# Kernel optimization log

Hardware: AMD Instinct MI355X
Metric: run time of the kernel (lower is better)

Reference implementation:

```python
import jax, jax.numpy as jnp
import numpy as np

N_NODES = 100000
N_EDGES = 1600000
IN_DIM = 128
HID = 32
HEADS = 4
OUT_DIM = 32


def gat_conv(x, W, al, ar, b, src, dst, apply_elu):
    """DGL-style GATConv. x:[N,F_in], W:[F_in,H*D], al/ar/b:[H,D]."""
    N = x.shape[0]
    H, D = al.shape
    f = (x @ W).reshape(N, H, D)                      # projected features [N,H,D]
    el = jnp.sum(f * al, axis=-1)                     # [N,H]
    er = jnp.sum(f * ar, axis=-1)                     # [N,H]
    e = jax.nn.leaky_relu(el[src] + er[dst], 0.2)     # per-edge scores [E,H]
    # segment softmax over incoming edges of each dst node
    m = jax.ops.segment_max(e, dst, num_segments=N)   # [N,H]
    m = jnp.where(jnp.isfinite(m), m, 0.0)            # zero-in-degree safety
    w = jnp.exp(e - m[dst])                           # [E,H]
    s = jax.ops.segment_sum(w, dst, num_segments=N)   # [N,H]
    alpha = w / jnp.maximum(s[dst], 1e-9)             # [E,H]
    out = jax.ops.segment_sum(alpha[:, :, None] * f[src], dst, num_segments=N)  # [N,H,D]
    out = out + b
    if apply_elu:
        out = jax.nn.elu(out)
    return out


def setup_inputs() -> dict:
    key = jax.random.key(0)
    ks = jax.random.split(key, 16)
    sc = 0.05
    HD = HEADS * HID
    return {
        "x": jax.random.normal(ks[0], (N_NODES, IN_DIM), jnp.float32),
        "src": jax.random.randint(ks[1], (N_EDGES,), 0, N_NODES, jnp.int32),
        "dst": jax.random.randint(ks[2], (N_EDGES,), 0, N_NODES, jnp.int32),
        "W1": jax.random.normal(ks[3], (IN_DIM, HD), jnp.float32) * sc,
        "al1": jax.random.normal(ks[4], (HEADS, HID), jnp.float32) * sc,
        "ar1": jax.random.normal(ks[5], (HEADS, HID), jnp.float32) * sc,
        "b1": jnp.zeros((HEADS, HID), jnp.float32),
        "W2": jax.random.normal(ks[6], (HD, HD), jnp.float32) * sc,
        "al2": jax.random.normal(ks[7], (HEADS, HID), jnp.float32) * sc,
        "ar2": jax.random.normal(ks[8], (HEADS, HID), jnp.float32) * sc,
        "b2": jnp.zeros((HEADS, HID), jnp.float32),
        "W3": jax.random.normal(ks[9], (HD, OUT_DIM), jnp.float32) * sc,
        "al3": jax.random.normal(ks[10], (1, OUT_DIM), jnp.float32) * sc,
        "ar3": jax.random.normal(ks[11], (1, OUT_DIM), jnp.float32) * sc,
        "b3": jnp.zeros((1, OUT_DIM), jnp.float32),
    }


def reference(x, src, dst, W1, al1, ar1, b1, W2, al2, ar2, b2, W3, al3, ar3, b3):
    h = gat_conv(x, W1, al1, ar1, b1, src, dst, apply_elu=True)
    h = h.reshape(h.shape[0], -1)                     # concat heads [N, H*D]
    h = gat_conv(h, W2, al2, ar2, b2, src, dst, apply_elu=True)
    h = h.reshape(h.shape[0], -1)
    h = gat_conv(h, W3, al3, ar3, b3, src, dst, apply_elu=False)
    return h.squeeze(1)                               # [N, OUT_DIM]
```

## Files before the change

kernel.cpp:

```cpp
#include <hip/hip_runtime.h>
#include <hip/hip_bf16.h>

#define IN_DIM 128
#define HDIM 128

typedef __attribute__((ext_vector_type(8))) short bf16x8;
typedef __attribute__((ext_vector_type(4))) float f32x4;
typedef __attribute__((ext_vector_type(4))) unsigned short ushort4v;

__device__ __forceinline__ float bf2f(unsigned short h) {
  union { unsigned u; float f; } a; a.u = ((unsigned)h) << 16; return a.f;
}
__device__ __forceinline__ unsigned short f2bf(float x) {
  union { float f; unsigned u; } a; a.f = x;
  unsigned r = a.u + 0x7FFFu + ((a.u >> 16) & 1u);
  return (unsigned short)(r >> 16);
}
__device__ __forceinline__ void bfsplit(float x, unsigned short& h, unsigned short& l) {
  h = f2bf(x);
  l = f2bf(x - bf2f(h));
}


__global__ __launch_bounds__(256) void hist_kernel(const int* __restrict__ dst,
                                                   int* __restrict__ deg, int E) {
  int e = blockIdx.x * 256 + threadIdx.x;
  if (e < E) atomicAdd(&deg[dst[e]], 1);
}

__global__ __launch_bounds__(512) void scan1_kernel(const int* __restrict__ deg,
                                                    int* __restrict__ partial,
                                                    int* __restrict__ bsum, int n) {
  __shared__ int sm[512];
  int g = blockIdx.x * 512 + threadIdx.x;
  int v = (g < n) ? deg[g] : 0;
  sm[threadIdx.x] = v;
  __syncthreads();
  for (int off = 1; off < 512; off <<= 1) {
    int t = (threadIdx.x >= off) ? sm[threadIdx.x - off] : 0;
    __syncthreads();
    sm[threadIdx.x] += t;
    __syncthreads();
  }
  if (g < n) partial[g] = sm[threadIdx.x];
  if (threadIdx.x == 511) bsum[blockIdx.x] = sm[511];
}

__global__ __launch_bounds__(512) void scan2_kernel(int* __restrict__ bsum, int nblk) {
  __shared__ int sm[512];
  int v = (threadIdx.x < nblk) ? bsum[threadIdx.x] : 0;
  sm[threadIdx.x] = v;
  __syncthreads();
  for (int off = 1; off < 512; off <<= 1) {
    int t = (threadIdx.x >= off) ? sm[threadIdx.x - off] : 0;
    __syncthreads();
    sm[threadIdx.x] += t;
    __syncthreads();
  }
  if (threadIdx.x < nblk) bsum[threadIdx.x] = sm[threadIdx.x];
}

__global__ __launch_bounds__(512) void scanfix_kernel(const int* __restrict__ partial,
                                                      const int* __restrict__ bsum,
                                                      const int* __restrict__ deg,
                                                      int* __restrict__ row_ptr,
                                                      int* __restrict__ cursor, int n) {
  int g = blockIdx.x * 512 + threadIdx.x;
  if (g >= n) return;
  int off = (blockIdx.x > 0) ? bsum[blockIdx.x - 1] : 0;
  int incl = partial[g] + off;
  row_ptr[g + 1] = incl;
  cursor[g] = incl - deg[g];
  if (g == 0) row_ptr[0] = 0;
}

__global__ __launch_bounds__(256) void scatter_kernel(const int* __restrict__ src,
                                                      const int* __restrict__ dst,
                                                      int* __restrict__ cursor,
                                                      int* __restrict__ col, int E) {
  int e = blockIdx.x * 256 + threadIdx.x;
  if (e >= E) return;
  int d = dst[e];
  int p = atomicAdd(&cursor[d], 1);
  col[p] = src[e];
}


__global__ __launch_bounds__(256) void split_kernel(const float* __restrict__ x,
                                                    unsigned short* __restrict__ xhi,
                                                    unsigned short* __restrict__ xlo,
                                                    int total4) {
  int idx = blockIdx.x * 256 + threadIdx.x;
  if (idx >= total4) return;
  float4 v = *(const float4*)&x[(size_t)idx * 4];
  ushort4v h, l;
  unsigned short a, b;
  bfsplit(v.x, a, b); h.x = a; l.x = b;
  bfsplit(v.y, a, b); h.y = a; l.y = b;
  bfsplit(v.z, a, b); h.z = a; l.z = b;
  bfsplit(v.w, a, b); h.w = a; l.w = b;
  *(ushort4v*)&xhi[(size_t)idx * 4] = h;
  *(ushort4v*)&xlo[(size_t)idx * 4] = l;
}


__global__ __launch_bounds__(64) void wfrag_kernel(const float* __restrict__ W, int HD, int NB,
                                                   unsigned short* __restrict__ whi,
                                                   unsigned short* __restrict__ wlo) {
  int fb = blockIdx.x;
  int l = threadIdx.x;
  int kb = fb / NB, nb = fb % NB;
  unsigned short hi[8], lo[8];
#pragma unroll
  for (int j = 0; j < 8; ++j) {
    int k = kb * 32 + (l >> 4) * 8 + j;
    int c = nb * 16 + (l & 15);
    bfsplit(W[(size_t)k * HD + c], hi[j], lo[j]);
  }
  size_t off = ((size_t)fb * 64 + l) * 8;
#pragma unroll
  for (int j = 0; j < 8; ++j) { whi[off + j] = hi[j]; wlo[off + j] = lo[j]; }
}


__global__ __launch_bounds__(256) void gemm128_mfma_kernel(
    const unsigned short* __restrict__ xhi, const unsigned short* __restrict__ xlo,
    const unsigned short* __restrict__ whi, const unsigned short* __restrict__ wlo,
    const float* __restrict__ al, const float* __restrict__ ar,
    float* __restrict__ F, float* __restrict__ el, float* __restrict__ er, int n) {
  const int lane = threadIdx.x & 63;
  const int w = threadIdx.x >> 6;
  const int bm = blockIdx.x * 128;
  const int lr = lane & 15;
  const int lk = lane >> 4;

  f32x4 acc[2][8];
#pragma unroll
  for (int mf = 0; mf < 2; ++mf)
#pragma unroll
    for (int nb = 0; nb < 8; ++nb) acc[mf][nb] = (f32x4){0.f, 0.f, 0.f, 0.f};

  int arow[2];
#pragma unroll
  for (int mf = 0; mf < 2; ++mf) {
    int r = bm + w * 32 + mf * 16 + lr;
    arow[mf] = (r < n) ? r : (n - 1);
  }

  for (int kb = 0; kb < 4; ++kb) {
    bf16x8 ah[2], alo2[2];
#pragma unroll
    for (int mf = 0; mf < 2; ++mf) {
      size_t ab = (size_t)arow[mf] * 128 + kb * 32 + lk * 8;
      ah[mf] = *(const bf16x8*)(xhi + ab);
      alo2[mf] = *(const bf16x8*)(xlo + ab);
    }
#pragma unroll
    for (int nb = 0; nb < 8; ++nb) {
      size_t wb = ((size_t)(kb * 8 + nb) * 64 + lane) * 8;
      bf16x8 bh = *(const bf16x8*)(whi + wb);
      bf16x8 bl = *(const bf16x8*)(wlo + wb);
#pragma unroll
      for (int mf = 0; mf < 2; ++mf) {
        acc[mf][nb] = __builtin_amdgcn_mfma_f32_16x16x32_bf16(ah[mf], bh, acc[mf][nb], 0, 0, 0);
        acc[mf][nb] = __builtin_amdgcn_mfma_f32_16x16x32_bf16(ah[mf], bl, acc[mf][nb], 0, 0, 0);
        acc[mf][nb] = __builtin_amdgcn_mfma_f32_16x16x32_bf16(alo2[mf], bh, acc[mf][nb], 0, 0, 0);
      }
    }
  }

  float alv[4][2], arv[4][2];
#pragma unroll
  for (int hh = 0; hh < 4; ++hh)
#pragma unroll
    for (int p = 0; p < 2; ++p) {
      alv[hh][p] = al[hh * 32 + p * 16 + lr];
      arv[hh][p] = ar[hh * 32 + p * 16 + lr];
    }

#pragma unroll
  for (int mf = 0; mf < 2; ++mf) {
#pragma unroll
    for (int r = 0; r < 4; ++r) {
      int grow = bm + w * 32 + mf * 16 + lk * 4 + r;
      bool ok = grow < n;
      if (ok) {
#pragma unroll
        for (int nb = 0; nb < 8; ++nb)
          F[(size_t)grow * HDIM + nb * 16 + lr] = acc[mf][nb][r];
      }
#pragma unroll
      for (int hh = 0; hh < 4; ++hh) {
        float pl = acc[mf][2 * hh][r] * alv[hh][0] + acc[mf][2 * hh + 1][r] * alv[hh][1];
        float pr = acc[mf][2 * hh][r] * arv[hh][0] + acc[mf][2 * hh + 1][r] * arv[hh][1];
        pl += __shfl_xor(pl, 1); pl += __shfl_xor(pl, 2);
        pl += __shfl_xor(pl, 4); pl += __shfl_xor(pl, 8);
        pr += __shfl_xor(pr, 1); pr += __shfl_xor(pr, 2);
        pr += __shfl_xor(pr, 4); pr += __shfl_xor(pr, 8);
        if (ok && lr == 0) {
          el[grow * 4 + hh] = pl;
          er[grow * 4 + hh] = pr;
        }
      }
    }
  }
}


__global__ __launch_bounds__(256) void gemm_n32_kernel(const unsigned short* __restrict__ Xhi,
                                                       const unsigned short* __restrict__ Xlo,
                                                       const float* __restrict__ W,
                                                       const float* __restrict__ al,
                                                       const float* __restrict__ ar,
                                                       float* __restrict__ Fout,
                                                       float* __restrict__ el,
                                                       float* __restrict__ er, int n) {
  __shared__ float Xs[32][132];
  __shared__ float Ws[128][32];
  const int tid = threadIdx.x;
  const int row0 = blockIdx.x * 32;
#pragma unroll
  for (int jj = 0; jj < 4; ++jj) {
    int idx = tid + jj * 256;
    int r = idx >> 3;
    int c4 = (idx & 7) * 4;
    *(float4*)&Ws[r][c4] = *(const float4*)&W[(size_t)r * 32 + c4];
  }
#pragma unroll
  for (int jj = 0; jj < 4; ++jj) {
    int idx = tid + jj * 256;
    int r = idx >> 5;
    int c4 = (idx & 31) * 4;
    int row = row0 + r;
    if (row < n) {
      ushort4v h = *(const ushort4v*)&Xhi[(size_t)row * HDIM + c4];
      ushort4v l = *(const ushort4v*)&Xlo[(size_t)row * HDIM + c4];
      Xs[r][c4 + 0] = bf2f(h.x) + bf2f(l.x);
      Xs[r][c4 + 1] = bf2f(h.y) + bf2f(l.y);
      Xs[r][c4 + 2] = bf2f(h.z) + bf2f(l.z);
      Xs[r][c4 + 3] = bf2f(h.w) + bf2f(l.w);
    } else {
      Xs[r][c4 + 0] = 0.f; Xs[r][c4 + 1] = 0.f; Xs[r][c4 + 2] = 0.f; Xs[r][c4 + 3] = 0.f;
    }
  }
  __syncthreads();
  const int r = tid >> 3, cg = (tid & 7) * 4;
  float4 acc = make_float4(0.f, 0.f, 0.f, 0.f);
#pragma unroll 8
  for (int k = 0; k < 128; ++k) {
    float a = Xs[r][k];
    float4 b = *(const float4*)&Ws[k][cg];
    acc.x = fmaf(a, b.x, acc.x); acc.y = fmaf(a, b.y, acc.y);
    acc.z = fmaf(a, b.z, acc.z); acc.w = fmaf(a, b.w, acc.w);
  }
  int row = row0 + r;
  if (row < n) *(float4*)&Fout[(size_t)row * 32 + cg] = acc;
  float pl = acc.x * al[cg] + acc.y * al[cg + 1] + acc.z * al[cg + 2] + acc.w * al[cg + 3];
  float pr = acc.x * ar[cg] + acc.y * ar[cg + 1] + acc.z * ar[cg + 2] + acc.w * ar[cg + 3];
  pl += __shfl_xor(pl, 1); pl += __shfl_xor(pl, 2); pl += __shfl_xor(pl, 4);
  pr += __shfl_xor(pr, 1); pr += __shfl_xor(pr, 2); pr += __shfl_xor(pr, 4);
  if ((tid & 7) == 0 && row < n) { el[row] = pl; er[row] = pr; }
}


template <int H, int D, bool ELU, bool OSPLIT>
__global__ __launch_bounds__(256) void aggregate_kernel(const float* __restrict__ f,
                                                        const float* __restrict__ el,
                                                        const float* __restrict__ er,
                                                        const float* __restrict__ bias,
                                                        const int* __restrict__ row_ptr,
                                                        const int* __restrict__ col,
                                                        float* __restrict__ out,
                                                        unsigned short* __restrict__ ohi,
                                                        unsigned short* __restrict__ olo,
                                                        int n) {
  constexpr int F = H * D;
  constexpr int LPN = F / 4;
  constexpr int NPB = 256 / LPN;
  int node = blockIdx.x * NPB + threadIdx.x / LPN;
  int ll = threadIdx.x % LPN;
  if (node >= n) return;
  const int h = (4 * ll) / D;
  const float er_n = er[node * H + h];
  int beg = row_ptr[node], end = row_ptr[node + 1];

  float ssum = 0.f;
  float4 acc = make_float4(0.f, 0.f, 0.f, 0.f);

  constexpr int U = 8;
  int i = beg;
  for (; i + U <= end; i += U) {
    int s[U];
#pragma unroll
    for (int j = 0; j < U; ++j) s[j] = col[i + j];
    float4 fv[U];
#pragma unroll
    for (int j = 0; j < U; ++j) fv[j] = *(const float4*)&f[(size_t)s[j] * F + 4 * ll];
    float elv[U];
#pragma unroll
    for (int j = 0; j < U; ++j) elv[j] = el[s[j] * H + h];
#pragma unroll
    for (int j = 0; j < U; ++j) {
      float e = elv[j] + er_n;
      e = (e > 0.f) ? e : 0.2f * e;
      float wgt = __expf(e);
      ssum += wgt;
      acc.x = fmaf(wgt, fv[j].x, acc.x);
      acc.y = fmaf(wgt, fv[j].y, acc.y);
      acc.z = fmaf(wgt, fv[j].z, acc.z);
      acc.w = fmaf(wgt, fv[j].w, acc.w);
    }
  }
  for (; i < end; ++i) {
    int s = col[i];
    float e = el[s * H + h] + er_n;
    e = (e > 0.f) ? e : 0.2f * e;
    float wgt = __expf(e);
    float4 fv = *(const float4*)&f[(size_t)s * F + 4 * ll];
    ssum += wgt;
    acc.x = fmaf(wgt, fv.x, acc.x);
    acc.y = fmaf(wgt, fv.y, acc.y);
    acc.z = fmaf(wgt, fv.z, acc.z);
    acc.w = fmaf(wgt, fv.w, acc.w);
  }

  float inv = 1.f / fmaxf(ssum, 1e-9f);
  float4 bb = *(const float4*)&bias[4 * ll];
  float4 o;
  o.x = acc.x * inv + bb.x;
  o.y = acc.y * inv + bb.y;
  o.z = acc.z * inv + bb.z;
  o.w = acc.w * inv + bb.w;
  if (ELU) {
    o.x = (o.x > 0.f) ? o.x : (__expf(o.x) - 1.f);
    o.y = (o.y > 0.f) ? o.y : (__expf(o.y) - 1.f);
    o.z = (o.z > 0.f) ? o.z : (__expf(o.z) - 1.f);
    o.w = (o.w > 0.f) ? o.w : (__expf(o.w) - 1.f);
  }
  if (OSPLIT) {
    ushort4v hi, lo;
    unsigned short a, b;
    bfsplit(o.x, a, b); hi.x = a; lo.x = b;
    bfsplit(o.y, a, b); hi.y = a; lo.y = b;
    bfsplit(o.z, a, b); hi.z = a; lo.z = b;
    bfsplit(o.w, a, b); hi.w = a; lo.w = b;
    *(ushort4v*)&ohi[(size_t)node * F + 4 * ll] = hi;
    *(ushort4v*)&olo[(size_t)node * F + 4 * ll] = lo;
  } else {
    *(float4*)&out[(size_t)node * F + 4 * ll] = o;
  }
}


extern "C" void kernel_launch(void* const* d_in, const int* in_sizes, int n_in,
                              void* d_out, int out_size, void* d_ws, size_t ws_size,
                              hipStream_t stream) {
  const float* x   = (const float*)d_in[0];
  const int*   src = (const int*)d_in[1];
  const int*   dst = (const int*)d_in[2];
  const float* W1  = (const float*)d_in[3];
  const float* al1 = (const float*)d_in[4];
  const float* ar1 = (const float*)d_in[5];
  const float* b1  = (const float*)d_in[6];
  const float* W2  = (const float*)d_in[7];
  const float* al2 = (const float*)d_in[8];
  const float* ar2 = (const float*)d_in[9];
  const float* b2  = (const float*)d_in[10];
  const float* W3  = (const float*)d_in[11];
  const float* al3 = (const float*)d_in[12];
  const float* ar3 = (const float*)d_in[13];
  const float* b3  = (const float*)d_in[14];
  float* out = (float*)d_out;

  const int N = in_sizes[0] / IN_DIM;
  const int E = in_sizes[1];

  char* w = (char*)d_ws;
  size_t off = 0;
  auto alloc = [&](size_t bytes) -> void* {
    void* p = w + off;
    off += (bytes + 255) & ~(size_t)255;
    return p;
  };
  int*   deg     = (int*)alloc((size_t)N * 4);
  int*   row_ptr = (int*)alloc((size_t)(N + 1) * 4);
  int*   cursor  = (int*)alloc((size_t)N * 4);
  int*   bsum    = (int*)alloc(4096);
  int*   col     = (int*)alloc((size_t)E * 4);
  float* el      = (float*)alloc((size_t)N * 4 * 4);
  float* er      = (float*)alloc((size_t)N * 4 * 4);
  float* bufA    = (float*)alloc((size_t)N * 128 * 4);
  unsigned short* bhi = (unsigned short*)alloc((size_t)N * 128 * 2);
  unsigned short* blo = (unsigned short*)alloc((size_t)N * 128 * 2);
  unsigned short* w1hi = (unsigned short*)alloc(4 * 8 * 64 * 8 * 2);
  unsigned short* w1lo = (unsigned short*)alloc(4 * 8 * 64 * 8 * 2);
  unsigned short* w2hi = (unsigned short*)alloc(4 * 8 * 64 * 8 * 2);
  unsigned short* w2lo = (unsigned short*)alloc(4 * 8 * 64 * 8 * 2);

  wfrag_kernel<<<32, 64, 0, stream>>>(W1, HDIM, 8, w1hi, w1lo);
  wfrag_kernel<<<32, 64, 0, stream>>>(W2, HDIM, 8, w2hi, w2lo);
  split_kernel<<<(N * 128 / 4 + 255) / 256, 256, 0, stream>>>(x, bhi, blo, N * 128 / 4);

  hipMemsetAsync(deg, 0, (size_t)N * 4, stream);
  hist_kernel<<<(E + 255) / 256, 256, 0, stream>>>(dst, deg, E);
  int nblk = (N + 511) / 512;
  scan1_kernel<<<nblk, 512, 0, stream>>>(deg, cursor, bsum, N);
  scan2_kernel<<<1, 512, 0, stream>>>(bsum, nblk);
  scanfix_kernel<<<nblk, 512, 0, stream>>>(cursor, bsum, deg, row_ptr, cursor, N);
  scatter_kernel<<<(E + 255) / 256, 256, 0, stream>>>(src, dst, cursor, col, E);

  const int gb = (N + 127) / 128;
  gemm128_mfma_kernel<<<gb, 256, 0, stream>>>(bhi, blo, w1hi, w1lo, al1, ar1, bufA, el, er, N);
  aggregate_kernel<4, 32, true, true><<<(N + 7) / 8, 256, 0, stream>>>(
      bufA, el, er, b1, row_ptr, col, nullptr, bhi, blo, N);
  gemm128_mfma_kernel<<<gb, 256, 0, stream>>>(bhi, blo, w2hi, w2lo, al2, ar2, bufA, el, er, N);
  aggregate_kernel<4, 32, true, true><<<(N + 7) / 8, 256, 0, stream>>>(
      bufA, el, er, b2, row_ptr, col, nullptr, bhi, blo, N);
  gemm_n32_kernel<<<(N + 31) / 32, 256, 0, stream>>>(bhi, blo, W3, al3, ar3, bufA, el, er, N);
  aggregate_kernel<1, 32, false, false><<<(N + 31) / 32, 256, 0, stream>>>(
      bufA, el, er, b3, row_ptr, col, out, nullptr, nullptr, N);
}
```

Baseline: 726.9 us.

## Build CSR via two-level bucketed counting sort instead of global atomics

Replaces the per-node histogram, three-kernel scan and atomic scatter with a bucketed radix-style CSR build. Edges are first grouped into 512-node buckets using shared-memory histograms and local scans, then each bucket is finalized in shared memory to produce row_ptr and col. This removes most global atomics on random addresses and several launches. It also merges the two weight-fragment kernels into one launch. It adds a temporary E-sized buffer, and the packed record format assumes src fits in 23 bits and at most 256 buckets.

```diff
diff --git a/kernel.cpp b/kernel.cpp
--- a/kernel.cpp
+++ b/kernel.cpp
@@ -3,6 +3,11 @@
 
 #define IN_DIM 128
 #define HDIM 128
+
+#define BSH 9
+#define NBKT_MAX 256
+#define CHUNK 4096
+#define EPT 16
 
 typedef __attribute__((ext_vector_type(8))) short bf16x8;
 typedef __attribute__((ext_vector_type(4))) float f32x4;
@@ -22,67 +27,139 @@
 }
 
 
-__global__ __launch_bounds__(256) void hist_kernel(const int* __restrict__ dst,
-                                                   int* __restrict__ deg, int E) {
-  int e = blockIdx.x * 256 + threadIdx.x;
-  if (e < E) atomicAdd(&deg[dst[e]], 1);
-}
-
-__global__ __launch_bounds__(512) void scan1_kernel(const int* __restrict__ deg,
-                                                    int* __restrict__ partial,
-                                                    int* __restrict__ bsum, int n) {
-  __shared__ int sm[512];
-  int g = blockIdx.x * 512 + threadIdx.x;
-  int v = (g < n) ? deg[g] : 0;
-  sm[threadIdx.x] = v;
+__global__ __launch_bounds__(256) void bhist_kernel(const int* __restrict__ dst,
+                                                    int* __restrict__ bcnt, int E, int nbkt) {
+  __shared__ int h[NBKT_MAX];
+  for (int i = threadIdx.x; i < nbkt; i += 256) h[i] = 0;
+  __syncthreads();
+  int stride = gridDim.x * 256;
+  for (int e = blockIdx.x * 256 + threadIdx.x; e < E; e += stride)
+    atomicAdd(&h[dst[e] >> BSH], 1);
+  __syncthreads();
+  for (int i = threadIdx.x; i < nbkt; i += 256)
+    if (h[i]) atomicAdd(&bcnt[i], h[i]);
+}
+
+__global__ __launch_bounds__(256) void bscan_kernel(const int* __restrict__ bcnt,
+                                                    int* __restrict__ bbase,
+                                                    int* __restrict__ bcursor,
+                                                    int* __restrict__ row_ptr, int nbkt) {
+  __shared__ int sc[256];
+  int t = threadIdx.x;
+  int v = (t < nbkt) ? bcnt[t] : 0;
+  sc[t] = v;
+  __syncthreads();
+  for (int off = 1; off < 256; off <<= 1) {
+    int u = (t >= off) ? sc[t - off] : 0;
+    __syncthreads();
+    sc[t] += u;
+    __syncthreads();
+  }
+  if (t < nbkt) { bbase[t] = sc[t] - v; bcursor[t] = 0; }
+  if (t == 0) row_ptr[0] = 0;
+}
+
+__global__ __launch_bounds__(256) void bscatter_kernel(const int* __restrict__ src,
+                                                       const int* __restrict__ dst,
+                                                       const int* __restrict__ bbase,
+                                                       int* __restrict__ bcursor,
+                                                       unsigned int* __restrict__ tmp,
+                                                       int E, int nbkt) {
+  __shared__ int cnt[NBKT_MAX];
+  __shared__ int boff[NBKT_MAX];
+  __shared__ int gb[NBKT_MAX];
+  __shared__ int sc[256];
+  __shared__ unsigned int recs[CHUNK];
+  __shared__ unsigned char bkts[CHUNK];
+  const int t = threadIdx.x;
+  for (int i = t; i < nbkt; i += 256) cnt[i] = 0;
+  __syncthreads();
+  const int base = blockIdx.x * CHUNK;
+  unsigned int myrec[EPT];
+  unsigned short myr[EPT];
+  unsigned char myb[EPT];
+#pragma unroll
+  for (int i = 0; i < EPT; ++i) {
+    int e = base + t + i * 256;
+    if (e < E) {
+      int s = src[e], d = dst[e];
+      int b = d >> BSH;
+      myb[i] = (unsigned char)b;
+      myrec[i] = ((unsigned)s << BSH) | (unsigned)(d & ((1 << BSH) - 1));
+      myr[i] = (unsigned short)atomicAdd(&cnt[b], 1);
+    } else {
+      myb[i] = 0xFF;
+    }
+  }
+  __syncthreads();
+  int cv = (t < nbkt) ? cnt[t] : 0;
+  sc[t] = cv;
+  __syncthreads();
+  for (int off = 1; off < 256; off <<= 1) {
+    int u = (t >= off) ? sc[t - off] : 0;
+    __syncthreads();
+    sc[t] += u;
+    __syncthreads();
+  }
+  if (t < nbkt) boff[t] = sc[t] - cv;
+  __syncthreads();
+  if (t < nbkt && cv > 0) gb[t] = atomicAdd(&bcursor[t], cv);
+  __syncthreads();
+#pragma unroll
+  for (int i = 0; i < EPT; ++i) {
+    if (myb[i] != 0xFF) {
+      int p = boff[myb[i]] + (int)myr[i];
+      recs[p] = myrec[i];
+      bkts[p] = myb[i];
+    }
+  }
+  __syncthreads();
+  int total = sc[255];
+  for (int i = t; i < total; i += 256) {
+    int b = bkts[i];
+    tmp[bbase[b] + gb[b] + (i - boff[b])] = recs[i];
+  }
+}
+
+__global__ __launch_bounds__(512) void bfinal_kernel(const unsigned int* __restrict__ tmp,
+                                                     const int* __restrict__ bbase,
+                                                     const int* __restrict__ bcnt,
+                                                     int* __restrict__ row_ptr,
+                                                     int* __restrict__ col, int n) {
+  const int b = blockIdx.x;
+  const int base = bbase[b];
+  const int cnt = bcnt[b];
+  const int node0 = b << BSH;
+  __shared__ int ncnt[512];
+  __shared__ int sc2[512];
+  __shared__ int cur[512];
+  const int t = threadIdx.x;
+  ncnt[t] = 0;
+  __syncthreads();
+  for (int i = t; i < cnt; i += 512) {
+    unsigned rec = tmp[base + i];
+    atomicAdd(&ncnt[rec & ((1 << BSH) - 1)], 1);
+  }
+  __syncthreads();
+  int v = ncnt[t];
+  sc2[t] = v;
   __syncthreads();
   for (int off = 1; off < 512; off <<= 1) {
-    int t = (threadIdx.x >= off) ? sm[threadIdx.x - off] : 0;
+    int u = (t >= off) ? sc2[t - off] : 0;
     __syncthreads();
-    sm[threadIdx.x] += t;
+    sc2[t] += u;
     __syncthreads();
   }
-  if (g < n) partial[g] = sm[threadIdx.x];
-  if (threadIdx.x == 511) bsum[blockIdx.x] = sm[511];
-}
-
-__global__ __launch_bounds__(512) void scan2_kernel(int* __restrict__ bsum, int nblk) {
-  __shared__ int sm[512];
-  int v = (threadIdx.x < nblk) ? bsum[threadIdx.x] : 0;
-  sm[threadIdx.x] = v;
-  __syncthreads();
-  for (int off = 1; off < 512; off <<= 1) {
-    int t = (threadIdx.x >= off) ? sm[threadIdx.x - off] : 0;
-    __syncthreads();
-    sm[threadIdx.x] += t;
-    __syncthreads();
-  }
-  if (threadIdx.x < nblk) bsum[threadIdx.x] = sm[threadIdx.x];
-}
-
-__global__ __launch_bounds__(512) void scanfix_kernel(const int* __restrict__ partial,
-                                                      const int* __restrict__ bsum,
-                                                      const int* __restrict__ deg,
-                                                      int* __restrict__ row_ptr,
-                                                      int* __restrict__ cursor, int n) {
-  int g = blockIdx.x * 512 + threadIdx.x;
-  if (g >= n) return;
-  int off = (blockIdx.x > 0) ? bsum[blockIdx.x - 1] : 0;
-  int incl = partial[g] + off;
-  row_ptr[g + 1] = incl;
-  cursor[g] = incl - deg[g];
-  if (g == 0) row_ptr[0] = 0;
-}
-
-__global__ __launch_bounds__(256) void scatter_kernel(const int* __restrict__ src,
-                                                      const int* __restrict__ dst,
-                                                      int* __restrict__ cursor,
-                                                      int* __restrict__ col, int E) {
-  int e = blockIdx.x * 256 + threadIdx.x;
-  if (e >= E) return;
-  int d = dst[e];
-  int p = atomicAdd(&cursor[d], 1);
-  col[p] = src[e];
+  cur[t] = base + sc2[t] - v;
+  int node = node0 + t;
+  if (node < n) row_ptr[node + 1] = base + sc2[t];
+  __syncthreads();
+  for (int i = t; i < cnt; i += 512) {
+    unsigned rec = tmp[base + i];
+    int ln = rec & ((1 << BSH) - 1);
+    int p = atomicAdd(&cur[ln], 1);
+    col[p] = (int)(rec >> BSH);
+  }
 }
 
 
@@ -104,18 +181,24 @@
 }
 
 
-__global__ __launch_bounds__(64) void wfrag_kernel(const float* __restrict__ W, int HD, int NB,
-                                                   unsigned short* __restrict__ whi,
-                                                   unsigned short* __restrict__ wlo) {
-  int fb = blockIdx.x;
+__global__ __launch_bounds__(64) void wfrag_kernel(const float* __restrict__ W1,
+                                                   const float* __restrict__ W2,
+                                                   unsigned short* __restrict__ w1hi,
+                                                   unsigned short* __restrict__ w1lo,
+                                                   unsigned short* __restrict__ w2hi,
+                                                   unsigned short* __restrict__ w2lo) {
+  int fb = blockIdx.x & 31;
+  const float* W = (blockIdx.x < 32) ? W1 : W2;
+  unsigned short* whi = (blockIdx.x < 32) ? w1hi : w2hi;
+  unsigned short* wlo = (blockIdx.x < 32) ? w1lo : w2lo;
   int l = threadIdx.x;
-  int kb = fb / NB, nb = fb % NB;
+  int kb = fb >> 3, nb = fb & 7;
   unsigned short hi[8], lo[8];
 #pragma unroll
   for (int j = 0; j < 8; ++j) {
     int k = kb * 32 + (l >> 4) * 8 + j;
     int c = nb * 16 + (l & 15);
-    bfsplit(W[(size_t)k * HD + c], hi[j], lo[j]);
+    bfsplit(W[(size_t)k * HDIM + c], hi[j], lo[j]);
   }
   size_t off = ((size_t)fb * 64 + l) * 8;
 #pragma unroll
@@ -374,6 +457,7 @@
 
   const int N = in_sizes[0] / IN_DIM;
   const int E = in_sizes[1];
+  const int nbkt = (N + (1 << BSH) - 1) >> BSH;
 
   char* w = (char*)d_ws;
   size_t off = 0;
@@ -382,10 +466,11 @@
     off += (bytes + 255) & ~(size_t)255;
     return p;
   };
-  int*   deg     = (int*)alloc((size_t)N * 4);
+  int*   bcnt    = (int*)alloc((size_t)NBKT_MAX * 4);
+  int*   bbase   = (int*)alloc((size_t)NBKT_MAX * 4);
+  int*   bcursor = (int*)alloc((size_t)NBKT_MAX * 4);
   int*   row_ptr = (int*)alloc((size_t)(N + 1) * 4);
-  int*   cursor  = (int*)alloc((size_t)N * 4);
-  int*   bsum    = (int*)alloc(4096);
+  unsigned int* tmp = (unsigned int*)alloc((size_t)E * 4);
   int*   col     = (int*)alloc((size_t)E * 4);
   float* el      = (float*)alloc((size_t)N * 4 * 4);
   float* er      = (float*)alloc((size_t)N * 4 * 4);
@@ -397,17 +482,14 @@
   unsigned short* w2hi = (unsigned short*)alloc(4 * 8 * 64 * 8 * 2);
   unsigned short* w2lo = (unsigned short*)alloc(4 * 8 * 64 * 8 * 2);
 
-  wfrag_kernel<<<32, 64, 0, stream>>>(W1, HDIM, 8, w1hi, w1lo);
-  wfrag_kernel<<<32, 64, 0, stream>>>(W2, HDIM, 8, w2hi, w2lo);
+  wfrag_kernel<<<64, 64, 0, stream>>>(W1, W2, w1hi, w1lo, w2hi, w2lo);
   split_kernel<<<(N * 128 / 4 + 255) / 256, 256, 0, stream>>>(x, bhi, blo, N * 128 / 4);
 
-  hipMemsetAsync(deg, 0, (size_t)N * 4, stream);
-  hist_kernel<<<(E + 255) / 256, 256, 0, stream>>>(dst, deg, E);
-  int nblk = (N + 511) / 512;
-  scan1_kernel<<<nblk, 512, 0, stream>>>(deg, cursor, bsum, N);
-  scan2_kernel<<<1, 512, 0, stream>>>(bsum, nblk);
-  scanfix_kernel<<<nblk, 512, 0, stream>>>(cursor, bsum, deg, row_ptr, cursor, N);
-  scatter_kernel<<<(E + 255) / 256, 256, 0, stream>>>(src, dst, cursor, col, E);
+  hipMemsetAsync(bcnt, 0, (size_t)NBKT_MAX * 4, stream);
+  bhist_kernel<<<1024, 256, 0, stream>>>(dst, bcnt, E, nbkt);
+  bscan_kernel<<<1, 256, 0, stream>>>(bcnt, bbase, bcursor, row_ptr, nbkt);
+  bscatter_kernel<<<(E + CHUNK - 1) / CHUNK, 256, 0, stream>>>(src, dst, bbase, bcursor, tmp, E, nbkt);
+  bfinal_kernel<<<nbkt, 512, 0, stream>>>(tmp, bbase, bcnt, row_ptr, col, N);
 
   const int gb = (N + 127) / 128;
   gemm128_mfma_kernel<<<gb, 256, 0, stream>>>(bhi, blo, w1hi, w1lo, al1, ar1, bufA, el, er, N);
```

Result: faster. 593.8 us (-18.3%).
